# Optimization experiments

Measured on AMD Instinct MI355X. Metric: run time of the kernel, lower is better.

The kernel has to match this reference:

```python
import jax, jax.numpy as jnp
import numpy as np

N_NODES = 100000
N_EDGES = 1600000
IN_CH = 128
HID = 128
OUT_CH = 16
N_GRAPHS = 64


def setup_inputs() -> dict:
    key = jax.random.key(0)
    ks = jax.random.split(key, 8)
    x = jax.random.normal(ks[0], (N_NODES, IN_CH), dtype=jnp.float32)
    edge_index = jax.random.randint(ks[1], (2, N_EDGES), 0, N_NODES, dtype=jnp.int64)
    batch = jnp.sort(jax.random.randint(ks[2], (N_NODES,), 0, N_GRAPHS, dtype=jnp.int64))
    s1 = 1.0 / np.sqrt(IN_CH)
    s2 = 1.0 / np.sqrt(HID)
    W1 = jax.random.uniform(ks[3], (IN_CH, HID), jnp.float32, -s1, s1)
    b1 = jnp.zeros((HID,), jnp.float32)
    W2 = jax.random.uniform(ks[4], (HID, HID), jnp.float32, -s2, s2)
    b2 = jnp.zeros((HID,), jnp.float32)
    Wfc = jax.random.uniform(ks[5], (HID, OUT_CH), jnp.float32, -s2, s2)
    bfc = jax.random.uniform(ks[6], (OUT_CH,), jnp.float32, -s2, s2)
    return {"x": x, "W1": W1, "b1": b1, "W2": W2, "b2": b2,
            "Wfc": Wfc, "bfc": bfc, "edge_index": edge_index, "batch": batch}


def _gcn_conv(x, W, b, src, dst, deg_inv_sqrt, deg_inv):
    # GCNConv with self-loops: out = D^-1/2 (A+I) D^-1/2 (x W) + b
    h = x @ W                                   # [N, H]
    norm = deg_inv_sqrt[src] * deg_inv_sqrt[dst]  # [E]
    agg = jax.ops.segment_sum(h[src] * norm[:, None], dst, num_segments=N_NODES)
    # self-loop term: deg_inv_sqrt[i]^2 * h[i]
    return agg + h * deg_inv[:, None] + b


def reference(x, W1, b1, W2, b2, Wfc, bfc, edge_index, batch):
    src, dst = edge_index[0], edge_index[1]
    # degree including self-loop
    deg = jax.ops.segment_sum(jnp.ones((N_EDGES,), jnp.float32), dst, num_segments=N_NODES) + 1.0
    deg_inv_sqrt = jax.lax.rsqrt(deg)
    deg_inv = 1.0 / deg
    h = jax.nn.relu(_gcn_conv(x, W1, b1, src, dst, deg_inv_sqrt, deg_inv))
    h = jax.nn.relu(_gcn_conv(h, W2, b2, src, dst, deg_inv_sqrt, deg_inv))
    # global mean pool over graphs
    sums = jax.ops.segment_sum(h, batch, num_segments=N_GRAPHS)          # [G, H]
    counts = jax.ops.segment_sum(jnp.ones((N_NODES,), jnp.float32), batch, num_segments=N_GRAPHS)
    pooled = sums / jnp.maximum(counts, 1.0)[:, None]
    return pooled @ Wfc + bfc
```

## Files before the change

### kernel.cpp

```cpp
#include <hip/hip_runtime.h>
#include <math.h>

#define NN 100000
#define NE 1600000
#define CH 128
#define OUTC 16
#define NG 64

#define CBSH 9
#define NCB 196
#define CHK 8192
#define CAP 10240
#define MAXB 12288

typedef __attribute__((ext_vector_type(8))) short bf16x8;
typedef __attribute__((ext_vector_type(4))) float f32x4;

__device__ __forceinline__ unsigned short f2bf(float f) {
    union { float f; unsigned u; } v; v.f = f;
    unsigned r = v.u + 0x7FFF + ((v.u >> 16) & 1);
    return (unsigned short)(r >> 16);
}
__device__ __forceinline__ float bflo(unsigned u) {
    union { unsigned u; float f; } v; v.u = u << 16; return v.f;
}
__device__ __forceinline__ float bfhi(unsigned u) {
    union { unsigned u; float f; } v; v.u = u & 0xffff0000u; return v.f;
}

__global__ void k_prep(const float* __restrict__ W1, const float* __restrict__ W2,
                       unsigned short* __restrict__ wt1, unsigned short* __restrict__ wt2,
                       const int* __restrict__ batch, int* __restrict__ gptr,
                       int* __restrict__ gfill, float* __restrict__ pooled) {
    int i = blockIdx.x * 256 + threadIdx.x;
    if (i < CH * CH) {
        int k = i >> 7, n = i & 127;
        wt1[n * CH + k] = f2bf(W1[i]);
    } else if (i < 2 * CH * CH) {
        int j = i - CH * CH;
        int k = j >> 7, n = j & 127;
        wt2[n * CH + k] = f2bf(W2[j]);
    }
    if (i < NCB) gfill[i] = 0;
    if (i < NG * CH) pooled[i] = 0.f;
    if (i < NN) {
        int b = batch[i];
        int prev = (i == 0) ? -1 : batch[i - 1];
        for (int g = prev + 1; g <= b; g++) gptr[g] = i;
        if (i == NN - 1) {
            for (int g = b + 1; g <= NG; g++) gptr[g] = NN;
        }
    }
}

__global__ __launch_bounds__(1024) void k_passA(const int* __restrict__ src, const int* __restrict__ dst,
                        int* __restrict__ gfill, unsigned* __restrict__ ebuf) {
    __shared__ unsigned lbuf[CHK];
    __shared__ unsigned char lbyte[CHK];
    __shared__ int hcnt[NCB];
    __shared__ int hbase[256];
    __shared__ int goff[NCB];
    int t = threadIdx.x;
    if (t < NCB) hcnt[t] = 0;
    __syncthreads();
    int base = blockIdx.x * CHK;
    int cb[8], slot[8]; unsigned pk[8];
#pragma unroll
    for (int i = 0; i < 8; i++) {
        int e = base + i * 1024 + t;
        cb[i] = -1;
        if (e < NE) {
            int d = dst[e], s = src[e];
            cb[i] = d >> CBSH;
            pk[i] = ((unsigned)s << CBSH) | (unsigned)(d & 511);
            slot[i] = atomicAdd(&hcnt[cb[i]], 1);
        }
    }
    __syncthreads();
    if (t < 256) hbase[t] = (t < NCB) ? hcnt[t] : 0;
    __syncthreads();
    for (int off = 1; off < 256; off <<= 1) {
        int v = 0;
        if (t < 256 && t >= off) v = hbase[t - off];
        __syncthreads();
        if (t < 256) hbase[t] += v;
        __syncthreads();
    }
    if (t < NCB) {
        int c = hcnt[t];
        int g = c ? atomicAdd(&gfill[t], c) : 0;
        goff[t] = t * CAP + g - (hbase[t] - c);
    }
    __syncthreads();
#pragma unroll
    for (int i = 0; i < 8; i++) {
        if (cb[i] >= 0) {
            int pos = hbase[cb[i]] - hcnt[cb[i]] + slot[i];
            lbuf[pos] = pk[i];
            lbyte[pos] = (unsigned char)cb[i];
        }
    }
    __syncthreads();
    int total = min(NE - base, CHK);
    for (int p = t; p < total; p += 1024) {
        unsigned v = lbuf[p];
        int b = lbyte[p];
        ebuf[goff[b] + p] = v;
    }
}

__global__ __launch_bounds__(1024) void k_passB(const unsigned* __restrict__ ebuf, const int* __restrict__ gfill,
                        int* __restrict__ degi, int* __restrict__ rowst,
                        float* __restrict__ dis, int* __restrict__ csr) {
    __shared__ int cnt[512];
    __shared__ int nbase[512];
    __shared__ int fill[512];
    __shared__ int stage[MAXB];
    int t = threadIdx.x;
    int cb = blockIdx.x;
    int nb0 = cb << CBSH;
    int ncnt = min(512, NN - nb0);
    int e0 = cb * CAP;
    int e1 = e0 + gfill[cb];
    if (t < 512) { cnt[t] = 0; fill[t] = 0; }
    __syncthreads();
    for (int e = e0 + t; e < e1; e += 1024)
        atomicAdd(&cnt[ebuf[e] & 511], 1);
    __syncthreads();
    if (t < 512) nbase[t] = cnt[t];
    __syncthreads();
    for (int off = 1; off < 512; off <<= 1) {
        int v = 0;
        if (t < 512 && t >= off) v = nbase[t - off];
        __syncthreads();
        if (t < 512) nbase[t] += v;
        __syncthreads();
    }
    for (int e = e0 + t; e < e1; e += 1024) {
        unsigned v = ebuf[e];
        int local = v & 511;
        int s = atomicAdd(&fill[local], 1);
        stage[nbase[local] - cnt[local] + s] = (int)(v >> CBSH);
    }
    __syncthreads();
    int total = e1 - e0;
    for (int p = t; p < total; p += 1024) csr[e0 + p] = stage[p];
    if (t < ncnt) {
        int c = cnt[t];
        degi[nb0 + t] = c;
        rowst[nb0 + t] = e0 + nbase[t] - c;
        dis[nb0 + t] = rsqrtf((float)c + 1.0f);
    }
}

template<bool F32IN>
__launch_bounds__(256, 2)
__global__ void k_gemm(const void* __restrict__ Av,
                       const unsigned short* __restrict__ WT,
                       const float* __restrict__ dis,
                       unsigned short* __restrict__ out) {
    int tid = threadIdx.x;
    int wave = tid >> 6, lane = tid & 63;
    int quad = lane >> 4, l16 = lane & 15;

    int rbase = blockIdx.x * 128 + wave * 32;

    bf16x8 af[2][4];
#pragma unroll
    for (int s = 0; s < 2; s++) {
        int row = rbase + s * 16 + l16;
        if (row >= NN) row = NN - 1;
        if (F32IN) {
            const float* arow = (const float*)Av + (size_t)row * CH + quad * 8;
#pragma unroll
            for (int ks = 0; ks < 4; ks++) {
                float4 lo = *(const float4*)(arow + ks * 32);
                float4 hi = *(const float4*)(arow + ks * 32 + 4);
                union { bf16x8 v; unsigned short u[8]; } tmp;
                tmp.u[0] = f2bf(lo.x); tmp.u[1] = f2bf(lo.y);
                tmp.u[2] = f2bf(lo.z); tmp.u[3] = f2bf(lo.w);
                tmp.u[4] = f2bf(hi.x); tmp.u[5] = f2bf(hi.y);
                tmp.u[6] = f2bf(hi.z); tmp.u[7] = f2bf(hi.w);
                af[s][ks] = tmp.v;
            }
        } else {
            const unsigned short* arow = (const unsigned short*)Av + (size_t)row * CH + quad * 8;
#pragma unroll
            for (int ks = 0; ks < 4; ks++) af[s][ks] = *(const bf16x8*)(arow + ks * 32);
        }
    }

    f32x4 acc[2][8];
#pragma unroll
    for (int s = 0; s < 2; s++)
#pragma unroll
        for (int t = 0; t < 8; t++) acc[s][t] = (f32x4){0.f, 0.f, 0.f, 0.f};

#pragma unroll
    for (int t = 0; t < 8; t++) {
        const unsigned short* wcol = WT + (size_t)(t * 16 + l16) * CH + quad * 8;
        bf16x8 b0 = *(const bf16x8*)(wcol);
        bf16x8 b1 = *(const bf16x8*)(wcol + 32);
        bf16x8 b2 = *(const bf16x8*)(wcol + 64);
        bf16x8 b3 = *(const bf16x8*)(wcol + 96);
#pragma unroll
        for (int s = 0; s < 2; s++) {
            acc[s][t] = __builtin_amdgcn_mfma_f32_16x16x32_bf16(af[s][0], b0, acc[s][t], 0, 0, 0);
            acc[s][t] = __builtin_amdgcn_mfma_f32_16x16x32_bf16(af[s][1], b1, acc[s][t], 0, 0, 0);
            acc[s][t] = __builtin_amdgcn_mfma_f32_16x16x32_bf16(af[s][2], b2, acc[s][t], 0, 0, 0);
            acc[s][t] = __builtin_amdgcn_mfma_f32_16x16x32_bf16(af[s][3], b3, acc[s][t], 0, 0, 0);
        }
    }

#pragma unroll
    for (int s = 0; s < 2; s++) {
#pragma unroll
        for (int r = 0; r < 4; r++) {
            int orow = rbase + s * 16 + quad * 4 + r;
            if (orow < NN) {
                float d = dis[orow];
#pragma unroll
                for (int t = 0; t < 8; t++) {
                    out[(size_t)orow * CH + t * 16 + l16] = f2bf(acc[s][t][r] * d);
                }
            }
        }
    }
}

__global__ void k_agg(const unsigned short* __restrict__ ht, const int* __restrict__ rowst,
                      const int* __restrict__ degi, const int* __restrict__ csr,
                      const float* __restrict__ dis, const float* __restrict__ bias,
                      unsigned short* __restrict__ out) {
    int wave = threadIdx.x >> 6;
    int lane = threadIdx.x & 63;
    int n = blockIdx.x * 4 + wave;
    if (n >= NN) return;
    const unsigned* base = (const unsigned*)ht;
    unsigned sv = base[(size_t)n * 64 + lane];
    float a0[8], a1[8];
    a0[0] = bflo(sv); a1[0] = bfhi(sv);
#pragma unroll
    for (int u = 1; u < 8; u++) { a0[u] = 0.f; a1[u] = 0.f; }
    int start = __builtin_amdgcn_readfirstlane(rowst[n]);
    int c = __builtin_amdgcn_readfirstlane(degi[n]);
    int j = 0;
    for (; j + 7 < c; j += 8) {
        int idx[8];
#pragma unroll
        for (int u = 0; u < 8; u++) idx[u] = csr[start + j + u];
        unsigned v[8];
#pragma unroll
        for (int u = 0; u < 8; u++) v[u] = base[(size_t)idx[u] * 64 + lane];
#pragma unroll
        for (int u = 0; u < 8; u++) { a0[u] += bflo(v[u]); a1[u] += bfhi(v[u]); }
    }
    for (; j < c; j++) {
        unsigned v0 = base[(size_t)csr[start + j] * 64 + lane];
        a0[j & 7] += bflo(v0); a1[j & 7] += bfhi(v0);
    }
#pragma unroll
    for (int off = 4; off >= 1; off >>= 1)
#pragma unroll
        for (int u = 0; u < off; u++) { a0[u] += a0[u + off]; a1[u] += a1[u + off]; }
    float d = dis[n];
    float bb0 = bias[lane * 2], bb1 = bias[lane * 2 + 1];
    float ox = fmaxf(fmaf(d, a0[0], bb0), 0.f);
    float oy = fmaxf(fmaf(d, a1[0], bb1), 0.f);
    unsigned pk = ((unsigned)f2bf(oy) << 16) | (unsigned)f2bf(ox);
    ((unsigned*)out)[(size_t)n * 64 + lane] = pk;
}

__global__ __launch_bounds__(1024) void k_aggpool(const unsigned short* __restrict__ ht,
                        const int* __restrict__ rowst, const int* __restrict__ degi,
                        const int* __restrict__ csr, const float* __restrict__ dis,
                        const float* __restrict__ bias, const int* __restrict__ batch,
                        float* __restrict__ pooled) {
    int wave = threadIdx.x >> 6;
    int lane = threadIdx.x & 63;
    int n = blockIdx.x * 16 + wave;
    const unsigned* base = (const unsigned*)ht;
    unsigned sv = base[(size_t)n * 64 + lane];
    float a0[8], a1[8];
    a0[0] = bflo(sv); a1[0] = bfhi(sv);
#pragma unroll
    for (int u = 1; u < 8; u++) { a0[u] = 0.f; a1[u] = 0.f; }
    int start = __builtin_amdgcn_readfirstlane(rowst[n]);
    int c = __builtin_amdgcn_readfirstlane(degi[n]);
    int j = 0;
    for (; j + 7 < c; j += 8) {
        int idx[8];
#pragma unroll
        for (int u = 0; u < 8; u++) idx[u] = csr[start + j + u];
        unsigned v[8];
#pragma unroll
        for (int u = 0; u < 8; u++) v[u] = base[(size_t)idx[u] * 64 + lane];
#pragma unroll
        for (int u = 0; u < 8; u++) { a0[u] += bflo(v[u]); a1[u] += bfhi(v[u]); }
    }
    for (; j < c; j++) {
        unsigned v0 = base[(size_t)csr[start + j] * 64 + lane];
        a0[j & 7] += bflo(v0); a1[j & 7] += bfhi(v0);
    }
#pragma unroll
    for (int off = 4; off >= 1; off >>= 1)
#pragma unroll
        for (int u = 0; u < off; u++) { a0[u] += a0[u + off]; a1[u] += a1[u + off]; }
    float d = dis[n];
    float bb0 = bias[lane * 2], bb1 = bias[lane * 2 + 1];
    float ox = fmaxf(fmaf(d, a0[0], bb0), 0.f);
    float oy = fmaxf(fmaf(d, a1[0], bb1), 0.f);

    ox = bflo((unsigned)f2bf(ox));
    oy = bflo((unsigned)f2bf(oy));

    int g = batch[n];
    int g0 = batch[blockIdx.x * 16];
    int g15 = batch[blockIdx.x * 16 + 15];
    if (g0 == g15) {
        __shared__ float sred[2][16][64];
        sred[0][wave][lane] = ox; sred[1][wave][lane] = oy;
        __syncthreads();
#pragma unroll
        for (int off = 8; off >= 1; off >>= 1) {
            if (wave < off) {
                sred[0][wave][lane] += sred[0][wave + off][lane];
                sred[1][wave][lane] += sred[1][wave + off][lane];
            }
            __syncthreads();
        }
        if (wave == 0) {
            atomicAdd(&pooled[g0 * CH + lane * 2],     sred[0][0][lane]);
            atomicAdd(&pooled[g0 * CH + lane * 2 + 1], sred[1][0][lane]);
        }
    } else {
        atomicAdd(&pooled[g * CH + lane * 2],     ox);
        atomicAdd(&pooled[g * CH + lane * 2 + 1], oy);
    }
}

__global__ void k_final(const float* __restrict__ pooled, const int* __restrict__ gptr,
                        const float* __restrict__ Wfc, const float* __restrict__ bfc,
                        float* __restrict__ out) {
    int idx = blockIdx.x * 256 + threadIdx.x;
    if (idx >= NG * OUTC) return;
    int g = idx >> 4, o = idx & 15;
    float c = (float)(gptr[g + 1] - gptr[g]);
    float inv = 1.0f / fmaxf(c, 1.0f);
    float s = 0.f;
    for (int k = 0; k < CH; k++) s += pooled[g * CH + k] * Wfc[k * OUTC + o];
    out[idx] = fmaf(s, inv, bfc[o]);
}

extern "C" void kernel_launch(void* const* d_in, const int* in_sizes, int n_in,
                              void* d_out, int out_size, void* d_ws, size_t ws_size,
                              hipStream_t stream) {
    (void)in_sizes; (void)n_in; (void)out_size; (void)ws_size;
    const float* x   = (const float*)d_in[0];
    const float* W1  = (const float*)d_in[1];
    const float* b1  = (const float*)d_in[2];
    const float* W2  = (const float*)d_in[3];
    const float* b2  = (const float*)d_in[4];
    const float* Wfc = (const float*)d_in[5];
    const float* bfc = (const float*)d_in[6];
    const int* ei    = (const int*)d_in[7];
    const int* batch = (const int*)d_in[8];
    const int* esrc = ei;
    const int* edst = ei + NE;
    float* out = (float*)d_out;

    char* w = (char*)d_ws;
    unsigned short* bufA = (unsigned short*)w; w += (size_t)NN * CH * 2;
    unsigned short* bufB = (unsigned short*)w; w += (size_t)NN * CH * 2;
    unsigned short* wt1  = (unsigned short*)w; w += (size_t)CH * CH * 2;
    unsigned short* wt2  = (unsigned short*)w; w += (size_t)CH * CH * 2;
    unsigned* ebuf = (unsigned*)w; w += (size_t)NCB * CAP * 4;
    int* csr    = (int*)w;    w += (size_t)NCB * CAP * 4;
    int* degi   = (int*)w;    w += (size_t)NN * 4;
    int* rowst  = (int*)w;    w += (size_t)NN * 4;
    float* dis  = (float*)w;  w += (size_t)NN * 4;
    int* gfill  = (int*)w;    w += NCB * 4;
    int* gptr   = (int*)w;    w += (NG + 1) * 4;
    float* pooled = (float*)w; w += (size_t)NG * CH * 4;

    const int sortBlocks = (NE + CHK - 1) / CHK;
    const int gemmBlocks = (NN + 127) / 128;

    k_prep<<<(NN + 255) / 256, 256, 0, stream>>>(W1, W2, wt1, wt2, batch, gptr, gfill, pooled);
    k_passA<<<sortBlocks, 1024, 0, stream>>>(esrc, edst, gfill, ebuf);
    k_passB<<<NCB, 1024, 0, stream>>>(ebuf, gfill, degi, rowst, dis, csr);

    k_gemm<true><<<gemmBlocks, 256, 0, stream>>>(x, wt1, dis, bufA);
    k_agg<<<NN / 4, 256, 0, stream>>>(bufA, rowst, degi, csr, dis, b1, bufB);
    k_gemm<false><<<gemmBlocks, 256, 0, stream>>>(bufB, wt2, dis, bufA);
    k_aggpool<<<NN / 16, 1024, 0, stream>>>(bufA, rowst, degi, csr, dis, b2, batch, pooled);

    k_final<<<(NG * OUTC + 255) / 256, 256, 0, stream>>>(pooled, gptr, Wfc, bfc, out);
}
```

Before: 328.9 us.

## Fuse layer-1 aggregation with layer-2 GEMM and per-wave pooling accumulation

The first aggregation is merged into the second GEMM: each wave aggregates 32 nodes into an LDS tile, then the block runs MFMA on that tile, which removes the bf16 round trip of the intermediate through global memory and one launch. The pooling kernel now gives each wave 32 consecutive nodes and keeps running per-graph sums in registers, issuing atomics only when the graph changes. In exchange, parallelism drops sharply: only about 782 blocks of 256 threads, with each wave walking 32 nodes serially. That could hurt latency hiding for the gather-bound aggregation.

```diff
diff --git a/kernel.cpp b/kernel.cpp
--- a/kernel.cpp
+++ b/kernel.cpp
@@ -12,6 +12,7 @@
 #define CHK 8192
 #define CAP 10240
 #define MAXB 12288
+#define LDSW 68
 
 typedef __attribute__((ext_vector_type(8))) short bf16x8;
 typedef __attribute__((ext_vector_type(4))) float f32x4;
@@ -26,6 +27,42 @@
 }
 __device__ __forceinline__ float bfhi(unsigned u) {
     union { unsigned u; float f; } v; v.u = u & 0xffff0000u; return v.f;
+}
+
+__device__ __forceinline__ float2 node_agg(const unsigned* __restrict__ base,
+        const int* __restrict__ rowst, const int* __restrict__ degi,
+        const int* __restrict__ csr, const float* __restrict__ dis,
+        float bb0, float bb1, int n, int lane) {
+    unsigned sv = base[(size_t)n * 64 + lane];
+    float a0[8], a1[8];
+    a0[0] = bflo(sv); a1[0] = bfhi(sv);
+#pragma unroll
+    for (int u = 1; u < 8; u++) { a0[u] = 0.f; a1[u] = 0.f; }
+    int start = __builtin_amdgcn_readfirstlane(rowst[n]);
+    int c = __builtin_amdgcn_readfirstlane(degi[n]);
+    int j = 0;
+    for (; j + 7 < c; j += 8) {
+        int idx[8];
+#pragma unroll
+        for (int u = 0; u < 8; u++) idx[u] = csr[start + j + u];
+        unsigned v[8];
+#pragma unroll
+        for (int u = 0; u < 8; u++) v[u] = base[(size_t)idx[u] * 64 + lane];
+#pragma unroll
+        for (int u = 0; u < 8; u++) { a0[u] += bflo(v[u]); a1[u] += bfhi(v[u]); }
+    }
+    for (; j < c; j++) {
+        unsigned v0 = base[(size_t)csr[start + j] * 64 + lane];
+        a0[j & 7] += bflo(v0); a1[j & 7] += bfhi(v0);
+    }
+#pragma unroll
+    for (int off = 4; off >= 1; off >>= 1)
+#pragma unroll
+        for (int u = 0; u < off; u++) { a0[u] += a0[u + off]; a1[u] += a1[u + off]; }
+    float d = dis[n];
+    float ox = fmaxf(fmaf(d, a0[0], bb0), 0.f);
+    float oy = fmaxf(fmaf(d, a1[0], bb1), 0.f);
+    return make_float2(ox, oy);
 }
 
 __global__ void k_prep(const float* __restrict__ W1, const float* __restrict__ W2,
@@ -153,12 +190,11 @@
     }
 }
 
-template<bool F32IN>
 __launch_bounds__(256, 2)
-__global__ void k_gemm(const void* __restrict__ Av,
-                       const unsigned short* __restrict__ WT,
-                       const float* __restrict__ dis,
-                       unsigned short* __restrict__ out) {
+__global__ void k_gemm1(const float* __restrict__ A,
+                        const unsigned short* __restrict__ WT,
+                        const float* __restrict__ dis,
+                        unsigned short* __restrict__ out) {
     int tid = threadIdx.x;
     int wave = tid >> 6, lane = tid & 63;
     int quad = lane >> 4, l16 = lane & 15;
@@ -170,23 +206,17 @@
     for (int s = 0; s < 2; s++) {
         int row = rbase + s * 16 + l16;
         if (row >= NN) row = NN - 1;
-        if (F32IN) {
-            const float* arow = (const float*)Av + (size_t)row * CH + quad * 8;
-#pragma unroll
-            for (int ks = 0; ks < 4; ks++) {
-                float4 lo = *(const float4*)(arow + ks * 32);
-                float4 hi = *(const float4*)(arow + ks * 32 + 4);
-                union { bf16x8 v; unsigned short u[8]; } tmp;
-                tmp.u[0] = f2bf(lo.x); tmp.u[1] = f2bf(lo.y);
-                tmp.u[2] = f2bf(lo.z); tmp.u[3] = f2bf(lo.w);
-                tmp.u[4] = f2bf(hi.x); tmp.u[5] = f2bf(hi.y);
-                tmp.u[6] = f2bf(hi.z); tmp.u[7] = f2bf(hi.w);
-                af[s][ks] = tmp.v;
-            }
-        } else {
-            const unsigned short* arow = (const unsigned short*)Av + (size_t)row * CH + quad * 8;
-#pragma unroll
-            for (int ks = 0; ks < 4; ks++) af[s][ks] = *(const bf16x8*)(arow + ks * 32);
+        const float* arow = A + (size_t)row * CH + quad * 8;
+#pragma unroll
+        for (int ks = 0; ks < 4; ks++) {
+            float4 lo = *(const float4*)(arow + ks * 32);
+            float4 hi = *(const float4*)(arow + ks * 32 + 4);
+            union { bf16x8 v; unsigned short u[8]; } tmp;
+            tmp.u[0] = f2bf(lo.x); tmp.u[1] = f2bf(lo.y);
+            tmp.u[2] = f2bf(lo.z); tmp.u[3] = f2bf(lo.w);
+            tmp.u[4] = f2bf(hi.x); tmp.u[5] = f2bf(hi.y);
+            tmp.u[6] = f2bf(hi.z); tmp.u[7] = f2bf(hi.w);
+            af[s][ks] = tmp.v;
         }
     }
 
@@ -228,115 +258,103 @@
     }
 }
 
-__global__ void k_agg(const unsigned short* __restrict__ ht, const int* __restrict__ rowst,
-                      const int* __restrict__ degi, const int* __restrict__ csr,
-                      const float* __restrict__ dis, const float* __restrict__ bias,
-                      unsigned short* __restrict__ out) {
+__launch_bounds__(256)
+__global__ void k_aggemm(const unsigned short* __restrict__ bufA,
+                         const int* __restrict__ rowst, const int* __restrict__ degi,
+                         const int* __restrict__ csr, const float* __restrict__ dis,
+                         const float* __restrict__ b1,
+                         const unsigned short* __restrict__ WT,
+                         unsigned short* __restrict__ out) {
+    __shared__ unsigned hs[128 * LDSW];
+    int tid = threadIdx.x;
+    int wave = tid >> 6, lane = tid & 63;
+    int quad = lane >> 4, l16 = lane & 15;
+    int rbase = blockIdx.x * 128 + wave * 32;
+    const unsigned* base = (const unsigned*)bufA;
+    float bb0 = b1[lane * 2], bb1 = b1[lane * 2 + 1];
+
+    for (int i = 0; i < 32; i++) {
+        int n = rbase + i;
+        int nc = n < NN ? n : NN - 1;
+        float2 o = node_agg(base, rowst, degi, csr, dis, bb0, bb1, nc, lane);
+        unsigned pk = ((unsigned)f2bf(o.y) << 16) | (unsigned)f2bf(o.x);
+        hs[(wave * 32 + i) * LDSW + lane] = pk;
+    }
+    __syncthreads();
+
+    bf16x8 af[2][4];
+#pragma unroll
+    for (int s = 0; s < 2; s++) {
+        int r = wave * 32 + s * 16 + l16;
+#pragma unroll
+        for (int ks = 0; ks < 4; ks++)
+            af[s][ks] = *(const bf16x8*)&hs[r * LDSW + quad * 4 + ks * 16];
+    }
+
+    f32x4 acc[2][8];
+#pragma unroll
+    for (int s = 0; s < 2; s++)
+#pragma unroll
+        for (int t = 0; t < 8; t++) acc[s][t] = (f32x4){0.f, 0.f, 0.f, 0.f};
+
+#pragma unroll
+    for (int t = 0; t < 8; t++) {
+        const unsigned short* wcol = WT + (size_t)(t * 16 + l16) * CH + quad * 8;
+        bf16x8 b0 = *(const bf16x8*)(wcol);
+        bf16x8 b1f = *(const bf16x8*)(wcol + 32);
+        bf16x8 b2f = *(const bf16x8*)(wcol + 64);
+        bf16x8 b3f = *(const bf16x8*)(wcol + 96);
+#pragma unroll
+        for (int s = 0; s < 2; s++) {
+            acc[s][t] = __builtin_amdgcn_mfma_f32_16x16x32_bf16(af[s][0], b0,  acc[s][t], 0, 0, 0);
+            acc[s][t] = __builtin_amdgcn_mfma_f32_16x16x32_bf16(af[s][1], b1f, acc[s][t], 0, 0, 0);
+            acc[s][t] = __builtin_amdgcn_mfma_f32_16x16x32_bf16(af[s][2], b2f, acc[s][t], 0, 0, 0);
+            acc[s][t] = __builtin_amdgcn_mfma_f32_16x16x32_bf16(af[s][3], b3f, acc[s][t], 0, 0, 0);
+        }
+    }
+
+#pragma unroll
+    for (int s = 0; s < 2; s++) {
+#pragma unroll
+        for (int r = 0; r < 4; r++) {
+            int orow = rbase + s * 16 + quad * 4 + r;
+            if (orow < NN) {
+                float d = dis[orow];
+#pragma unroll
+                for (int t = 0; t < 8; t++) {
+                    out[(size_t)orow * CH + t * 16 + l16] = f2bf(acc[s][t][r] * d);
+                }
+            }
+        }
+    }
+}
+
+__global__ void k_aggpool(const unsigned short* __restrict__ ht,
+                          const int* __restrict__ rowst, const int* __restrict__ degi,
+                          const int* __restrict__ csr, const float* __restrict__ dis,
+                          const float* __restrict__ b2, const int* __restrict__ batch,
+                          float* __restrict__ pooled) {
     int wave = threadIdx.x >> 6;
     int lane = threadIdx.x & 63;
-    int n = blockIdx.x * 4 + wave;
-    if (n >= NN) return;
+    int n0 = (blockIdx.x * 4 + wave) * 32;
+    if (n0 >= NN) return;
+    int n1 = n0 + 32; if (n1 > NN) n1 = NN;
     const unsigned* base = (const unsigned*)ht;
-    unsigned sv = base[(size_t)n * 64 + lane];
-    float a0[8], a1[8];
-    a0[0] = bflo(sv); a1[0] = bfhi(sv);
-#pragma unroll
-    for (int u = 1; u < 8; u++) { a0[u] = 0.f; a1[u] = 0.f; }
-    int start = __builtin_amdgcn_readfirstlane(rowst[n]);
-    int c = __builtin_amdgcn_readfirstlane(degi[n]);
-    int j = 0;
-    for (; j + 7 < c; j += 8) {
-        int idx[8];
-#pragma unroll
-        for (int u = 0; u < 8; u++) idx[u] = csr[start + j + u];
-        unsigned v[8];
-#pragma unroll
-        for (int u = 0; u < 8; u++) v[u] = base[(size_t)idx[u] * 64 + lane];
-#pragma unroll
-        for (int u = 0; u < 8; u++) { a0[u] += bflo(v[u]); a1[u] += bfhi(v[u]); }
-    }
-    for (; j < c; j++) {
-        unsigned v0 = base[(size_t)csr[start + j] * 64 + lane];
-        a0[j & 7] += bflo(v0); a1[j & 7] += bfhi(v0);
-    }
-#pragma unroll
-    for (int off = 4; off >= 1; off >>= 1)
-#pragma unroll
-        for (int u = 0; u < off; u++) { a0[u] += a0[u + off]; a1[u] += a1[u + off]; }
-    float d = dis[n];
-    float bb0 = bias[lane * 2], bb1 = bias[lane * 2 + 1];
-    float ox = fmaxf(fmaf(d, a0[0], bb0), 0.f);
-    float oy = fmaxf(fmaf(d, a1[0], bb1), 0.f);
-    unsigned pk = ((unsigned)f2bf(oy) << 16) | (unsigned)f2bf(ox);
-    ((unsigned*)out)[(size_t)n * 64 + lane] = pk;
-}
-
-__global__ __launch_bounds__(1024) void k_aggpool(const unsigned short* __restrict__ ht,
-                        const int* __restrict__ rowst, const int* __restrict__ degi,
-                        const int* __restrict__ csr, const float* __restrict__ dis,
-                        const float* __restrict__ bias, const int* __restrict__ batch,
-                        float* __restrict__ pooled) {
-    int wave = threadIdx.x >> 6;
-    int lane = threadIdx.x & 63;
-    int n = blockIdx.x * 16 + wave;
-    const unsigned* base = (const unsigned*)ht;
-    unsigned sv = base[(size_t)n * 64 + lane];
-    float a0[8], a1[8];
-    a0[0] = bflo(sv); a1[0] = bfhi(sv);
-#pragma unroll
-    for (int u = 1; u < 8; u++) { a0[u] = 0.f; a1[u] = 0.f; }
-    int start = __builtin_amdgcn_readfirstlane(rowst[n]);
-    int c = __builtin_amdgcn_readfirstlane(degi[n]);
-    int j = 0;
-    for (; j + 7 < c; j += 8) {
-        int idx[8];
-#pragma unroll
-        for (int u = 0; u < 8; u++) idx[u] = csr[start + j + u];
-        unsigned v[8];
-#pragma unroll
-        for (int u = 0; u < 8; u++) v[u] = base[(size_t)idx[u] * 64 + lane];
-#pragma unroll
-        for (int u = 0; u < 8; u++) { a0[u] += bflo(v[u]); a1[u] += bfhi(v[u]); }
-    }
-    for (; j < c; j++) {
-        unsigned v0 = base[(size_t)csr[start + j] * 64 + lane];
-        a0[j & 7] += bflo(v0); a1[j & 7] += bfhi(v0);
-    }
-#pragma unroll
-    for (int off = 4; off >= 1; off >>= 1)
-#pragma unroll
-        for (int u = 0; u < off; u++) { a0[u] += a0[u + off]; a1[u] += a1[u + off]; }
-    float d = dis[n];
-    float bb0 = bias[lane * 2], bb1 = bias[lane * 2 + 1];
-    float ox = fmaxf(fmaf(d, a0[0], bb0), 0.f);
-    float oy = fmaxf(fmaf(d, a1[0], bb1), 0.f);
-
-    ox = bflo((unsigned)f2bf(ox));
-    oy = bflo((unsigned)f2bf(oy));
-
-    int g = batch[n];
-    int g0 = batch[blockIdx.x * 16];
-    int g15 = batch[blockIdx.x * 16 + 15];
-    if (g0 == g15) {
-        __shared__ float sred[2][16][64];
-        sred[0][wave][lane] = ox; sred[1][wave][lane] = oy;
-        __syncthreads();
-#pragma unroll
-        for (int off = 8; off >= 1; off >>= 1) {
-            if (wave < off) {
-                sred[0][wave][lane] += sred[0][wave + off][lane];
-                sred[1][wave][lane] += sred[1][wave + off][lane];
-            }
-            __syncthreads();
-        }
-        if (wave == 0) {
-            atomicAdd(&pooled[g0 * CH + lane * 2],     sred[0][0][lane]);
-            atomicAdd(&pooled[g0 * CH + lane * 2 + 1], sred[1][0][lane]);
-        }
-    } else {
-        atomicAdd(&pooled[g * CH + lane * 2],     ox);
-        atomicAdd(&pooled[g * CH + lane * 2 + 1], oy);
-    }
+    float bb0 = b2[lane * 2], bb1 = b2[lane * 2 + 1];
+    float p0 = 0.f, p1 = 0.f;
+    int gcur = __builtin_amdgcn_readfirstlane(batch[n0]);
+    for (int n = n0; n < n1; n++) {
+        int g = __builtin_amdgcn_readfirstlane(batch[n]);
+        if (g != gcur) {
+            atomicAdd(&pooled[gcur * CH + lane * 2],     p0);
+            atomicAdd(&pooled[gcur * CH + lane * 2 + 1], p1);
+            p0 = 0.f; p1 = 0.f; gcur = g;
+        }
+        float2 o = node_agg(base, rowst, degi, csr, dis, bb0, bb1, n, lane);
+        p0 += o.x; p1 += o.y;
+    }
+    atomicAdd(&pooled[gcur * CH + lane * 2],     p0);
+    atomicAdd(&pooled[gcur * CH + lane * 2 + 1], p1);
 }
 
 __global__ void k_final(const float* __restrict__ pooled, const int* __restrict__ gptr,
@@ -384,16 +402,15 @@
     float* pooled = (float*)w; w += (size_t)NG * CH * 4;
 
     const int sortBlocks = (NE + CHK - 1) / CHK;
-    const int gemmBlocks = (NN + 127) / 128;
+    const int rowBlocks  = (NN + 127) / 128;
 
     k_prep<<<(NN + 255) / 256, 256, 0, stream>>>(W1, W2, wt1, wt2, batch, gptr, gfill, pooled);
     k_passA<<<sortBlocks, 1024, 0, stream>>>(esrc, edst, gfill, ebuf);
     k_passB<<<NCB, 1024, 0, stream>>>(ebuf, gfill, degi, rowst, dis, csr);
 
-    k_gemm<true><<<gemmBlocks, 256, 0, stream>>>(x, wt1, dis, bufA);
-    k_agg<<<NN / 4, 256, 0, stream>>>(bufA, rowst, degi, csr, dis, b1, bufB);
-    k_gemm<false><<<gemmBlocks, 256, 0, stream>>>(bufB, wt2, dis, bufA);
-    k_aggpool<<<NN / 16, 1024, 0, stream>>>(bufA, rowst, degi, csr, dis, b2, batch, pooled);
+    k_gemm1<<<rowBlocks, 256, 0, stream>>>(x, wt1, dis, bufA);
+    k_aggemm<<<rowBlocks, 256, 0, stream>>>(bufA, rowst, degi, csr, dis, b1, wt2, bufB);
+    k_aggpool<<<rowBlocks, 256, 0, stream>>>(bufB, rowst, degi, csr, dis, b2, batch, pooled);
 
     k_final<<<(NG * OUTC + 255) / 256, 256, 0, stream>>>(pooled, gptr, Wfc, bfc, out);
 }
```

Result: slower. 386.2 us (+17.4%).
